# Kernel tuning notes

Hardware: AMD Instinct MI355X
Metric: run time of the kernel (lower is better)

## Reference

```python
import jax, jax.numpy as jnp
import numpy as np

N_DOCS = 500000
N_WORDS = 100000
EMB = 128
B = 16384
CTX = 8
K = 6


def setup_inputs() -> dict:
    key = jax.random.key(0)
    k1, k2, k3, k4, k5, k6 = jax.random.split(key, 6)
    D = jax.random.normal(k1, (N_DOCS, EMB), dtype=jnp.float32)
    # W = cat(randn(n_words, d), zeros(1, d)) -> last row is padding
    W = jax.random.normal(k2, (N_WORDS + 1, EMB), dtype=jnp.float32)
    W = W.at[-1].set(0.0)
    Wp = jax.random.normal(k3, (EMB, N_WORDS), dtype=jnp.float32)
    ctx_ids = jax.random.randint(k4, (B, CTX), 0, N_WORDS + 1, dtype=jnp.int64)
    doc_ids = jax.random.randint(k5, (B,), 0, N_DOCS, dtype=jnp.int64)
    target_and_noise_ids = jax.random.randint(k6, (B, K), 0, N_WORDS, dtype=jnp.int64)
    return {
        "D": D,
        "W": W,
        "Wp": Wp,
        "ctx_ids": ctx_ids,
        "doc_ids": doc_ids,
        "target_and_noise_ids": target_and_noise_ids,
    }


def reference(D, W, Wp, ctx_ids, doc_ids, target_and_noise_ids):
    # x[b] = D[doc_ids[b]] + sum_c W[ctx_ids[b, c]]      -> [B, d]
    x = D[doc_ids] + jnp.sum(W[ctx_ids], axis=1)
    # out[b, k] = x[b] . Wp[:, target_and_noise_ids[b, k]]
    # Wp.T[ids] gathers rows of Wp.T -> [B, K, d]
    out = jnp.einsum("bd,bkd->bk", x, Wp.T[target_and_noise_ids])
    return out
```

## Files before the change

kernel.cpp:

```cpp
#include <hip/hip_runtime.h>

#define N_DOCS 500000
#define N_WORDS 100000
#define EMB 128
#define BATCH 16384
#define CTX 8
#define K 6
#define TW 64
#define LSTRIDE 67
#define NTB ((N_WORDS + TW - 1) / TW)

__device__ __forceinline__ unsigned f2bf(float f) {
    unsigned u = __float_as_uint(f);
    unsigned r = u + 0x7fffu + ((u >> 16) & 1u);
    return r >> 16;
}
#define BF2F(h) __uint_as_float(((unsigned)(h)) << 16)

__global__ __launch_bounds__(256) void transpose_bf16(const float* __restrict__ Wp,
                                                      unsigned short* __restrict__ WpT) {
    __shared__ float tile[EMB * LSTRIDE];
    const int t = threadIdx.x;
    const int w0 = blockIdx.x * TW;

    {
        const int fq = t & 15, e0 = t >> 4;
        const int col = w0 + 4 * fq;
        if (col + 3 < N_WORDS) {
#pragma unroll
            for (int j = 0; j < 8; ++j) {
                const int e = e0 + 16 * j;
                const float4 v = *(const float4*)(Wp + (size_t)e * N_WORDS + col);
                float* d = &tile[e * LSTRIDE + 4 * fq];
                d[0] = v.x; d[1] = v.y; d[2] = v.z; d[3] = v.w;
            }
        }
    }
    __syncthreads();

#pragma unroll
    for (int r = 0; r < 4; ++r) {
        const int wl = 16 * r + (t >> 4);
        const int w = w0 + wl;
        if (w < N_WORDS) {
            const int db = 8 * (t & 15);
            float c[8];
#pragma unroll
            for (int j = 0; j < 8; ++j) c[j] = tile[(db + j) * LSTRIDE + wl];
            uint4 o;
            o.x = f2bf(c[0]) | (f2bf(c[1]) << 16);
            o.y = f2bf(c[2]) | (f2bf(c[3]) << 16);
            o.z = f2bf(c[4]) | (f2bf(c[5]) << 16);
            o.w = f2bf(c[6]) | (f2bf(c[7]) << 16);
            *(uint4*)(WpT + (size_t)w * EMB + db) = o;
        }
    }
}

__global__ __launch_bounds__(256) void nce_fused(const float* __restrict__ D,
                                                 const float* __restrict__ W,
                                                 const unsigned short* __restrict__ WpT,
                                                 const int* __restrict__ ctx_ids,
                                                 const int* __restrict__ doc_ids,
                                                 const int* __restrict__ tn_ids,
                                                 float* __restrict__ out) {
    const int lane = threadIdx.x & 63;
    const int b = __builtin_amdgcn_readfirstlane(blockIdx.x * 4 + (threadIdx.x >> 6));

    const int doc = doc_ids[b];
    float2 xx = ((const float2*)(D + (size_t)doc * EMB))[lane];
#pragma unroll
    for (int c = 0; c < CTX; ++c) {
        const int id = ctx_ids[b * CTX + c];
        const float2 w2 = ((const float2*)(W + (size_t)id * EMB))[lane];
        xx.x += w2.x;
        xx.y += w2.y;
    }

#pragma unroll
    for (int k = 0; k < K; ++k) {
        const int id = tn_ids[b * K + k];
        const ushort2 w2 = ((const ushort2*)(WpT + (size_t)id * EMB))[lane];
        float s = xx.x * BF2F(w2.x) + xx.y * BF2F(w2.y);
#pragma unroll
        for (int off = 32; off > 0; off >>= 1) s += __shfl_xor(s, off, 64);
        if (lane == 0) out[b * K + k] = s;
    }
}

__global__ __launch_bounds__(256) void nce_direct(
    const float* __restrict__ D, const float* __restrict__ W,
    const float* __restrict__ Wp, const int* __restrict__ ctx_ids,
    const int* __restrict__ doc_ids, const int* __restrict__ tn_ids,
    float* __restrict__ out) {
    const int wave = threadIdx.x >> 6, lane = threadIdx.x & 63;
    const int b = blockIdx.x * 4 + wave;
    if (b >= BATCH) return;
    float2 xx = ((const float2*)(D + (size_t)doc_ids[b] * EMB))[lane];
#pragma unroll
    for (int c = 0; c < CTX; ++c) {
        const float2 w2 = ((const float2*)(W + (size_t)ctx_ids[b * CTX + c] * EMB))[lane];
        xx.x += w2.x;
        xx.y += w2.y;
    }
#pragma unroll
    for (int k = 0; k < K; ++k) {
        const int id = tn_ids[b * K + k];
        float s = xx.x * Wp[(size_t)(2 * lane) * N_WORDS + id] +
                  xx.y * Wp[(size_t)(2 * lane + 1) * N_WORDS + id];
#pragma unroll
        for (int off = 32; off > 0; off >>= 1) s += __shfl_down(s, off, 64);
        if (lane == 0) out[b * K + k] = s;
    }
}

extern "C" void kernel_launch(void* const* d_in, const int* in_sizes, int n_in,
                              void* d_out, int out_size, void* d_ws, size_t ws_size,
                              hipStream_t stream) {
    const float* D  = (const float*)d_in[0];
    const float* W  = (const float*)d_in[1];
    const float* Wp = (const float*)d_in[2];
    const int* ctx  = (const int*)d_in[3];
    const int* doc  = (const int*)d_in[4];
    const int* tn   = (const int*)d_in[5];
    float* out = (float*)d_out;

    const size_t need = (size_t)N_WORDS * EMB * sizeof(unsigned short);
    if (ws_size >= need) {
        unsigned short* WpT = (unsigned short*)d_ws;
        transpose_bf16<<<NTB, 256, 0, stream>>>(Wp, WpT);
        nce_fused<<<BATCH / 4, 256, 0, stream>>>(D, W, WpT, ctx, doc, tn, out);
    } else {
        nce_direct<<<BATCH / 4, 256, 0, stream>>>(D, W, Wp, ctx, doc, tn, out);
    }
}
```

Measured before the change: 36.17 us.

## Map four batch rows per wavefront with 16-lane groups and wide loads

```diff
diff --git a/kernel.cpp b/kernel.cpp
--- a/kernel.cpp
+++ b/kernel.cpp
@@ -57,34 +57,55 @@
     }
 }
 
-__global__ __launch_bounds__(256) void nce_fused(const float* __restrict__ D,
-                                                 const float* __restrict__ W,
-                                                 const unsigned short* __restrict__ WpT,
-                                                 const int* __restrict__ ctx_ids,
-                                                 const int* __restrict__ doc_ids,
-                                                 const int* __restrict__ tn_ids,
-                                                 float* __restrict__ out) {
-    const int lane = threadIdx.x & 63;
-    const int b = __builtin_amdgcn_readfirstlane(blockIdx.x * 4 + (threadIdx.x >> 6));
+__global__ __launch_bounds__(256) void nce_fused4(const float* __restrict__ D,
+                                                  const float* __restrict__ W,
+                                                  const unsigned short* __restrict__ WpT,
+                                                  const int* __restrict__ ctx_ids,
+                                                  const int* __restrict__ doc_ids,
+                                                  const int* __restrict__ tn_ids,
+                                                  float* __restrict__ out) {
+    const int t = threadIdx.x;
+    const int lane = t & 63;
+    const int li = lane & 15;
+    const int b = blockIdx.x * 16 + (t >> 6) * 4 + (lane >> 4);
 
     const int doc = doc_ids[b];
-    float2 xx = ((const float2*)(D + (size_t)doc * EMB))[lane];
+    int cids[CTX];
+#pragma unroll
+    for (int c = 0; c < CTX; ++c) cids[c] = ctx_ids[b * CTX + c];
+    int ids[K];
+#pragma unroll
+    for (int k = 0; k < K; ++k) ids[k] = tn_ids[b * K + k];
+
+    const float* Dr = D + (size_t)doc * EMB + li * 8;
+    float4 a0 = *(const float4*)Dr;
+    float4 a1 = *(const float4*)(Dr + 4);
 #pragma unroll
     for (int c = 0; c < CTX; ++c) {
-        const int id = ctx_ids[b * CTX + c];
-        const float2 w2 = ((const float2*)(W + (size_t)id * EMB))[lane];
-        xx.x += w2.x;
-        xx.y += w2.y;
+        const float* Wr = W + (size_t)cids[c] * EMB + li * 8;
+        const float4 w0 = *(const float4*)Wr;
+        const float4 w1 = *(const float4*)(Wr + 4);
+        a0.x += w0.x; a0.y += w0.y; a0.z += w0.z; a0.w += w0.w;
+        a1.x += w1.x; a1.y += w1.y; a1.z += w1.z; a1.w += w1.w;
     }
+
+    uint4 wf[K];
+#pragma unroll
+    for (int k = 0; k < K; ++k)
+        wf[k] = *(const uint4*)(WpT + (size_t)ids[k] * EMB + li * 8);
 
 #pragma unroll
     for (int k = 0; k < K; ++k) {
-        const int id = tn_ids[b * K + k];
-        const ushort2 w2 = ((const ushort2*)(WpT + (size_t)id * EMB))[lane];
-        float s = xx.x * BF2F(w2.x) + xx.y * BF2F(w2.y);
-#pragma unroll
-        for (int off = 32; off > 0; off >>= 1) s += __shfl_xor(s, off, 64);
-        if (lane == 0) out[b * K + k] = s;
+        const uint4 u = wf[k];
+        float s = BF2F(u.x & 0xffff) * a0.x + BF2F(u.x >> 16) * a0.y +
+                  BF2F(u.y & 0xffff) * a0.z + BF2F(u.y >> 16) * a0.w +
+                  BF2F(u.z & 0xffff) * a1.x + BF2F(u.z >> 16) * a1.y +
+                  BF2F(u.w & 0xffff) * a1.z + BF2F(u.w >> 16) * a1.w;
+        s += __shfl_xor(s, 8, 64);
+        s += __shfl_xor(s, 4, 64);
+        s += __shfl_xor(s, 2, 64);
+        s += __shfl_xor(s, 1, 64);
+        if (li == 0) out[b * K + k] = s;
     }
 }
 
@@ -129,7 +150,7 @@
     if (ws_size >= need) {
         unsigned short* WpT = (unsigned short*)d_ws;
         transpose_bf16<<<NTB, 256, 0, stream>>>(Wp, WpT);
-        nce_fused<<<BATCH / 4, 256, 0, stream>>>(D, W, WpT, ctx, doc, tn, out);
+        nce_fused4<<<BATCH / 16, 256, 0, stream>>>(D, W, WpT, ctx, doc, tn, out);
     } else {
         nce_direct<<<BATCH / 4, 256, 0, stream>>>(D, W, Wp, ctx, doc, tn, out);
     }
```

Result: faster. 34.26 us (-5.3%).
